# Kernel tuning notes

Hardware: AMD Instinct MI355X
Metric: run time of the kernel (lower is better)

Reference implementation:

```python
import jax, jax.numpy as jnp
import numpy as np

# XORChainModel.forward: state[0] = inputs[0]; state[i] = state[i-1] ^ inputs[i]
# i.e. a cumulative XOR (inclusive prefix scan with XOR) along the chain axis.
# XOR is associative, so we use jax.lax.associative_scan (log-depth parallel scan).

SEQ_LEN = 4096  # number of steps in the XOR chain (len(inputs) list in torch)
BITS = 8192     # self.bits: width of each bit vector


def setup_inputs() -> dict:
    key = jax.random.key(0)
    # inputs[i] is a 1-D bit vector of length BITS; stack the whole list into [S, BITS]
    inputs = jax.random.randint(key, (SEQ_LEN, BITS), 0, 2, dtype=jnp.int32)
    return {"inputs": inputs}


def reference(inputs):
    # outputs[i] = inputs[0] ^ inputs[1] ^ ... ^ inputs[i]
    # Equivalent to the torch module's list of per-step states, stacked on axis 0.
    return jax.lax.associative_scan(jnp.bitwise_xor, inputs, axis=0)
```

## Files before the change

### kernel.cpp

```cpp
#include <hip/hip_runtime.h>
#include <stdint.h>


#define S 4096
#define B4 2048
#define TPB 512
#define NCT (B4 / TPB)
#define OUTER 64
#define NOUT (S / OUTER)
#define NBLK (NOUT * NCT)
#define NWORDS (NOUT * B4)
#define POISON 0xAAAAAAAAu
#define STG 4
#define NSTG (OUTER / STG)

typedef unsigned int v4u __attribute__((ext_vector_type(4)));
typedef unsigned long long u64;
typedef const __attribute__((address_space(1))) v4u* gp1_t;
typedef __attribute__((address_space(3))) v4u* lp3_t;

__device__ __forceinline__ bool valid(unsigned w) {
    return (w & 0x300u) == 0x100u;
}
__device__ __forceinline__ u64 repl(unsigned nib) {
    u64 m = nib;
    m |= m << 4; m |= m << 8; m |= m << 16; m |= m << 32;
    return m;
}

__global__ __launch_bounds__(TPB) void xor_plainst(
        const v4u* __restrict__ in, v4u* __restrict__ out,
        unsigned* __restrict__ ctl) {
    unsigned* agg = ctl + 64;
    unsigned* inc = agg + NWORDS;

    __shared__ v4u sh[2][STG][TPB];

    const int tid   = (int)threadIdx.x;
    const int bid   = (int)blockIdx.x;
    const int ct    = bid & (NCT - 1);
    const int o     = bid >> 2;
    const int colg  = ct * TPB + tid;
    const int wbase = tid & ~63;

    const v4u* p = in + (size_t)o * OUTER * B4 + colg;

    auto STAGE = [&](int srow, int buf) {
#pragma unroll
        for (int j = 0; j < STG; ++j)
            __builtin_amdgcn_global_load_lds(
                (gp1_t)(const void*)(p + (size_t)(srow + j) * B4),
                (lp3_t)(void*)&sh[buf][j][wbase], 16, 0, 0);
    };

    u64 q[4] = {0ull, 0ull, 0ull, 0ull};
    STAGE(0, 0);
    STAGE(STG, 1);
#pragma unroll
    for (int s = 0; s < NSTG; ++s) {
        if (s < NSTG - 1) asm volatile("s_waitcnt vmcnt(4)" ::: "memory");
        else              asm volatile("s_waitcnt vmcnt(0)" ::: "memory");
        const int buf = s & 1;
#pragma unroll
        for (int j = 0; j < STG; ++j) {
            v4u v = sh[buf][j][tid];
            unsigned n = (v.x & 1u) | ((v.y & 1u) << 1) |
                         ((v.z & 1u) << 2) | ((v.w & 1u) << 3);
            const int r = s * STG + j;
            q[r >> 4] ^= (u64)n << (4 * (r & 15));
        }
        asm volatile("s_waitcnt lgkmcnt(0)" ::: "memory");
        if (s + 2 < NSTG) STAGE((s + 2) * STG, buf);
    }

    u64 tt = q[0] ^ q[1] ^ q[2] ^ q[3];
    tt ^= tt >> 32; tt ^= tt >> 16; tt ^= tt >> 8; tt ^= tt >> 4;
    const unsigned myagg = (unsigned)tt & 0xFu;
    __hip_atomic_store(&agg[(size_t)o * B4 + colg], 0x100u | myagg,
                       __ATOMIC_RELAXED, __HIP_MEMORY_SCOPE_AGENT);

    unsigned ex = 0u;
    int k = o - 1;
    while (k >= 0) {
        unsigned iw = __hip_atomic_load(&inc[(size_t)k * B4 + colg],
                                        __ATOMIC_RELAXED,
                                        __HIP_MEMORY_SCOPE_AGENT);
        if (valid(iw)) { ex ^= (iw & 0xFu); break; }
        int n = (k + 1 < 16) ? (k + 1) : 16;
        unsigned a[16];
        for (int j = 0; j < n; ++j)
            a[j] = __hip_atomic_load(&agg[(size_t)(k - j) * B4 + colg],
                                     __ATOMIC_RELAXED,
                                     __HIP_MEMORY_SCOPE_AGENT);
        int consumed = 0;
        for (int j = 0; j < n; ++j) {
            if (valid(a[j])) { ex ^= (a[j] & 0xFu); ++consumed; }
            else break;
        }
        k -= consumed;
        if (consumed == 0) __builtin_amdgcn_s_sleep(1);
    }
    __hip_atomic_store(&inc[(size_t)o * B4 + colg], 0x100u | (ex ^ myagg),
                       __ATOMIC_RELAXED, __HIP_MEMORY_SCOPE_AGENT);

    unsigned carry = ex;
    v4u* qo = out + (size_t)o * OUTER * B4 + colg;
#pragma unroll
    for (int kk = 0; kk < 4; ++kk) {
        u64 x = q[kk];
        x ^= x << 4; x ^= x << 8; x ^= x << 16; x ^= x << 32;
        const u64 f = x ^ repl(carry);
        carry ^= (unsigned)(x >> 60) & 0xFu;
#pragma unroll
        for (int j = 0; j < 16; ++j) {
            const unsigned n = (unsigned)(f >> (4 * j)) & 0xFu;
            v4u ov = (v4u){n & 1u, (n >> 1) & 1u, (n >> 2) & 1u, (n >> 3) & 1u};
            qo[(size_t)(kk * 16 + j) * B4] = ov;
        }
    }
}

extern "C" void kernel_launch(void* const* d_in, const int* in_sizes, int n_in,
                              void* d_out, int out_size, void* d_ws, size_t ws_size,
                              hipStream_t stream) {
    const v4u* in = (const v4u*)d_in[0];
    v4u* out = (v4u*)d_out;
    unsigned* ctl = (unsigned*)d_ws;

    xor_plainst<<<NBLK, TPB, 0, stream>>>(in, out, ctl);
}
```

Before: 239.7 us.

## Make blocks persistent over strided 16-row chunks and prefetch the next chunk during lookback

The kernel now launches a fixed grid of 256 blocks. Each block processes four 16-row chunks, strided by the group count, instead of one 64-row chunk per block. The loads for the next chunk are issued before the decoupled-lookback spin, so memory traffic overlaps the wait on predecessors. Output stores become nontemporal. The lookback chain gets four times longer (256 chunk aggregates per column), and it now depends on persistent blocks making forward progress in order, which could add serialization latency.

After: 251.1 us. 1.05x slower.

```diff
diff --git a/kernel.cpp b/kernel.cpp
--- a/kernel.cpp
+++ b/kernel.cpp
@@ -6,13 +6,14 @@
 #define B4 2048
 #define TPB 512
 #define NCT (B4 / TPB)
-#define OUTER 64
-#define NOUT (S / OUTER)
-#define NBLK (NOUT * NCT)
+#define PH 4
+#define CHROWS 16
+#define NOUT (S / CHROWS)
+#define NBLK 256
+#define GRP (NBLK / NCT)
 #define NWORDS (NOUT * B4)
-#define POISON 0xAAAAAAAAu
 #define STG 4
-#define NSTG (OUTER / STG)
+#define NSTG (CHROWS / STG)
 
 typedef unsigned int v4u __attribute__((ext_vector_type(4)));
 typedef unsigned long long u64;
@@ -28,7 +29,7 @@
     return m;
 }
 
-__global__ __launch_bounds__(TPB) void xor_plainst(
+__global__ __launch_bounds__(TPB) void xor_pipe(
         const v4u* __restrict__ in, v4u* __restrict__ out,
         unsigned* __restrict__ ctl) {
     unsigned* agg = ctl + 64;
@@ -39,84 +40,88 @@
     const int tid   = (int)threadIdx.x;
     const int bid   = (int)blockIdx.x;
     const int ct    = bid & (NCT - 1);
-    const int o     = bid >> 2;
+    const int g     = bid >> 2;
     const int colg  = ct * TPB + tid;
     const int wbase = tid & ~63;
 
-    const v4u* p = in + (size_t)o * OUTER * B4 + colg;
-
-    auto STAGE = [&](int srow, int buf) {
+    auto STAGE = [&](int grow, int buf) {
 #pragma unroll
         for (int j = 0; j < STG; ++j)
             __builtin_amdgcn_global_load_lds(
-                (gp1_t)(const void*)(p + (size_t)(srow + j) * B4),
+                (gp1_t)(const void*)(in + (size_t)(grow + j) * B4 + colg),
                 (lp3_t)(void*)&sh[buf][j][wbase], 16, 0, 0);
     };
 
-    u64 q[4] = {0ull, 0ull, 0ull, 0ull};
-    STAGE(0, 0);
-    STAGE(STG, 1);
+    int o = g;
+    STAGE(o * CHROWS, 0);
+    STAGE(o * CHROWS + STG, 1);
+
+    for (int i = 0; i < PH; ++i) {
+        u64 q = 0ull;
 #pragma unroll
-    for (int s = 0; s < NSTG; ++s) {
-        if (s < NSTG - 1) asm volatile("s_waitcnt vmcnt(4)" ::: "memory");
-        else              asm volatile("s_waitcnt vmcnt(0)" ::: "memory");
-        const int buf = s & 1;
+        for (int s = 0; s < NSTG; ++s) {
+            if (s < NSTG - 1) asm volatile("s_waitcnt vmcnt(4)" ::: "memory");
+            else              asm volatile("s_waitcnt vmcnt(0)" ::: "memory");
+            const int buf = s & 1;
 #pragma unroll
-        for (int j = 0; j < STG; ++j) {
-            v4u v = sh[buf][j][tid];
-            unsigned n = (v.x & 1u) | ((v.y & 1u) << 1) |
-                         ((v.z & 1u) << 2) | ((v.w & 1u) << 3);
-            const int r = s * STG + j;
-            q[r >> 4] ^= (u64)n << (4 * (r & 15));
+            for (int j = 0; j < STG; ++j) {
+                v4u v = sh[buf][j][tid];
+                unsigned n = (v.x & 1u) | ((v.y & 1u) << 1) |
+                             ((v.z & 1u) << 2) | ((v.w & 1u) << 3);
+                q ^= (u64)n << (4 * (s * STG + j));
+            }
+            asm volatile("s_waitcnt lgkmcnt(0)" ::: "memory");
+            if (s + 2 < NSTG) STAGE(o * CHROWS + (s + 2) * STG, buf);
         }
-        asm volatile("s_waitcnt lgkmcnt(0)" ::: "memory");
-        if (s + 2 < NSTG) STAGE((s + 2) * STG, buf);
-    }
 
-    u64 tt = q[0] ^ q[1] ^ q[2] ^ q[3];
-    tt ^= tt >> 32; tt ^= tt >> 16; tt ^= tt >> 8; tt ^= tt >> 4;
-    const unsigned myagg = (unsigned)tt & 0xFu;
-    __hip_atomic_store(&agg[(size_t)o * B4 + colg], 0x100u | myagg,
-                       __ATOMIC_RELAXED, __HIP_MEMORY_SCOPE_AGENT);
+        u64 tt = q;
+        tt ^= tt >> 32; tt ^= tt >> 16; tt ^= tt >> 8; tt ^= tt >> 4;
+        const unsigned myagg = (unsigned)tt & 0xFu;
+        __hip_atomic_store(&agg[(size_t)o * B4 + colg], 0x100u | myagg,
+                           __ATOMIC_RELAXED, __HIP_MEMORY_SCOPE_AGENT);
 
-    unsigned ex = 0u;
-    int k = o - 1;
-    while (k >= 0) {
-        unsigned iw = __hip_atomic_load(&inc[(size_t)k * B4 + colg],
-                                        __ATOMIC_RELAXED,
-                                        __HIP_MEMORY_SCOPE_AGENT);
-        if (valid(iw)) { ex ^= (iw & 0xFu); break; }
-        int n = (k + 1 < 16) ? (k + 1) : 16;
-        unsigned a[16];
-        for (int j = 0; j < n; ++j)
-            a[j] = __hip_atomic_load(&agg[(size_t)(k - j) * B4 + colg],
-                                     __ATOMIC_RELAXED,
-                                     __HIP_MEMORY_SCOPE_AGENT);
-        int consumed = 0;
-        for (int j = 0; j < n; ++j) {
-            if (valid(a[j])) { ex ^= (a[j] & 0xFu); ++consumed; }
-            else break;
+        const int onext = o + GRP;
+        if (i + 1 < PH) {
+            STAGE(onext * CHROWS, 0);
+            STAGE(onext * CHROWS + STG, 1);
         }
-        k -= consumed;
-        if (consumed == 0) __builtin_amdgcn_s_sleep(1);
-    }
-    __hip_atomic_store(&inc[(size_t)o * B4 + colg], 0x100u | (ex ^ myagg),
-                       __ATOMIC_RELAXED, __HIP_MEMORY_SCOPE_AGENT);
 
-    unsigned carry = ex;
-    v4u* qo = out + (size_t)o * OUTER * B4 + colg;
+        unsigned ex = 0u;
+        int k = o - 1;
+        while (k >= 0) {
+            unsigned iw = __hip_atomic_load(&inc[(size_t)k * B4 + colg],
+                                            __ATOMIC_RELAXED,
+                                            __HIP_MEMORY_SCOPE_AGENT);
+            if (valid(iw)) { ex ^= (iw & 0xFu); break; }
+            int n = (k + 1 < 16) ? (k + 1) : 16;
+            unsigned a[16];
+            for (int j = 0; j < n; ++j)
+                a[j] = __hip_atomic_load(&agg[(size_t)(k - j) * B4 + colg],
+                                         __ATOMIC_RELAXED,
+                                         __HIP_MEMORY_SCOPE_AGENT);
+            int consumed = 0;
+            for (int j = 0; j < n; ++j) {
+                if (valid(a[j])) { ex ^= (a[j] & 0xFu); ++consumed; }
+                else break;
+            }
+            k -= consumed;
+            if (consumed == 0) __builtin_amdgcn_s_sleep(1);
+        }
+        __hip_atomic_store(&inc[(size_t)o * B4 + colg], 0x100u | (ex ^ myagg),
+                           __ATOMIC_RELAXED, __HIP_MEMORY_SCOPE_AGENT);
+
+        u64 x = q;
+        x ^= x << 4; x ^= x << 8; x ^= x << 16; x ^= x << 32;
+        const u64 f = x ^ repl(ex);
+        v4u* qo = out + (size_t)o * CHROWS * B4 + colg;
 #pragma unroll
-    for (int kk = 0; kk < 4; ++kk) {
-        u64 x = q[kk];
-        x ^= x << 4; x ^= x << 8; x ^= x << 16; x ^= x << 32;
-        const u64 f = x ^ repl(carry);
-        carry ^= (unsigned)(x >> 60) & 0xFu;
-#pragma unroll
-        for (int j = 0; j < 16; ++j) {
+        for (int j = 0; j < CHROWS; ++j) {
             const unsigned n = (unsigned)(f >> (4 * j)) & 0xFu;
             v4u ov = (v4u){n & 1u, (n >> 1) & 1u, (n >> 2) & 1u, (n >> 3) & 1u};
-            qo[(size_t)(kk * 16 + j) * B4] = ov;
+            __builtin_nontemporal_store(ov, &qo[(size_t)j * B4]);
         }
+
+        o = onext;
     }
 }
 
@@ -127,5 +132,5 @@
     v4u* out = (v4u*)d_out;
     unsigned* ctl = (unsigned*)d_ws;
 
-    xor_plainst<<<NBLK, TPB, 0, stream>>>(in, out, ctl);
+    xor_pipe<<<NBLK, TPB, 0, stream>>>(in, out, ctl);
 }
```
